# Optimization experiments

Measured on AMD Instinct MI355X. Metric: run time of the kernel, lower is better.

## Reference

```python
import jax, jax.numpy as jnp
import numpy as np

EPS = 1e-06

def quant4(x):
    # per-row (last dim) symmetric 4-bit quant with straight-through estimator
    max_abs = jax.lax.stop_gradient(jnp.max(jnp.abs(x), axis=-1, keepdims=True))
    max_abs = jnp.maximum(max_abs, EPS)
    q = jnp.clip(jnp.round(x / max_abs * 7.0), -8.0, 7.0)
    deq = q * max_abs / 7.0
    # forward value = deq, gradient = identity w.r.t. x
    return x + jax.lax.stop_gradient(deq - x)

def ternary_weight(w):
    thresh = 0.05 * jnp.mean(jnp.abs(w))
    sign = jnp.where(jnp.abs(w) < thresh, 0.0, jnp.sign(w))
    alpha = jnp.mean(jnp.abs(w), axis=1, keepdims=True)  # per output row scale
    tern = sign * alpha
    # forward value = tern, gradient = identity w.r.t. w
    return w + jax.lax.stop_gradient(tern - w)

def setup_inputs() -> dict:
    key = jax.random.key(0)
    kx, kw = jax.random.split(key)
    B, S, IN_F, OUT_F = 8, 4096, 1024, 1024
    x = jax.random.normal(kx, (B, S, IN_F), dtype=jnp.float32)
    weight = jax.random.normal(kw, (OUT_F, IN_F), dtype=jnp.float32) / np.sqrt(IN_F)
    bias = jnp.zeros((OUT_F,), dtype=jnp.float32)
    return {"x": x, "weight": weight, "bias": bias}

def reference(x, weight, bias):
    xq = quant4(x)                       # [B, S, in_f]
    wq = ternary_weight(weight)          # [out_f, in_f]
    out = jnp.einsum('bsi,oi->bso', xq, wq) + bias
    return out
```

## Files before the change

kernel.cpp:

```cpp
#include <hip/hip_runtime.h>
#include <hip/hip_bf16.h>


typedef __attribute__((ext_vector_type(4))) int int32x4;
typedef __attribute__((ext_vector_type(4))) float f32x4;

#define IN_F 1024
#define OUT_F 1024

__device__ inline float waveMax(float v) {
#pragma unroll
    for (int off = 32; off > 0; off >>= 1) v = fmaxf(v, __shfl_xor(v, off, 64));
    return v;
}
__device__ inline float waveSum(float v) {
#pragma unroll
    for (int off = 32; off > 0; off >>= 1) v += __shfl_xor(v, off, 64);
    return v;
}

__device__ inline unsigned int pack4(int a, int b, int c, int d) {
    return (unsigned)(a & 255) | ((unsigned)(b & 255) << 8) |
           ((unsigned)(c & 255) << 16) | ((unsigned)(d & 255) << 24);
}

__global__ __launch_bounds__(256) void wsum_kernel(const float* __restrict__ w,
                                                   float* __restrict__ alpha) {
    __shared__ float red[4];
    const int row = blockIdx.x;
    const int tid = threadIdx.x;
    f32x4 v = reinterpret_cast<const f32x4*>(w + (size_t)row * IN_F)[tid];
    float s = fabsf(v.x) + fabsf(v.y) + fabsf(v.z) + fabsf(v.w);
    s = waveSum(s);
    if ((tid & 63) == 0) red[tid >> 6] = s;
    __syncthreads();
    if (tid == 0)
        alpha[row] = (red[0] + red[1] + red[2] + red[3]) * (1.0f / (float)IN_F);
}

__global__ __launch_bounds__(256) void wquant_kernel(const float* __restrict__ w,
                                                     const float* __restrict__ alpha,
                                                     signed char* __restrict__ wq) {
    __shared__ float red[4];
    const int tid = threadIdx.x;
    f32x4 a = reinterpret_cast<const f32x4*>(alpha)[tid];
    float s = a.x + a.y + a.z + a.w;
    s = waveSum(s);
    if ((tid & 63) == 0) red[tid >> 6] = s;
    __syncthreads();
    const float thresh =
        0.05f * ((red[0] + red[1] + red[2] + red[3]) * (1.0f / (float)OUT_F));

    const int row = blockIdx.x;
    f32x4 v = reinterpret_cast<const f32x4*>(w + (size_t)row * IN_F)[tid];
    int s0 = (fabsf(v.x) < thresh) ? 0 : (v.x > 0.0f ? 1 : -1);
    int s1 = (fabsf(v.y) < thresh) ? 0 : (v.y > 0.0f ? 1 : -1);
    int s2 = (fabsf(v.z) < thresh) ? 0 : (v.z > 0.0f ? 1 : -1);
    int s3 = (fabsf(v.w) < thresh) ? 0 : (v.w > 0.0f ? 1 : -1);
    reinterpret_cast<unsigned int*>(wq)[(size_t)row * (IN_F / 4) + tid] =
        pack4(s0, s1, s2, s3);
}

__global__ __launch_bounds__(256) void quantx_kernel(const float* __restrict__ x,
                                                     signed char* __restrict__ xq,
                                                     float* __restrict__ sx) {
    const int row = blockIdx.x * 4 + (threadIdx.x >> 6);
    const int lane = threadIdx.x & 63;
    const f32x4* xr = reinterpret_cast<const f32x4*>(x + (size_t)row * IN_F);

    f32x4 v[4];
    float m = 0.0f;
#pragma unroll
    for (int j = 0; j < 4; ++j) {
        v[j] = __builtin_nontemporal_load(&xr[lane + 64 * j]);
        m = fmaxf(m, fmaxf(fmaxf(fabsf(v[j].x), fabsf(v[j].y)),
                           fmaxf(fabsf(v[j].z), fabsf(v[j].w))));
    }
    m = waveMax(m);
    m = fmaxf(m, 1e-6f);

    unsigned int* xqr = reinterpret_cast<unsigned int*>(xq + (size_t)row * IN_F);
#pragma unroll
    for (int j = 0; j < 4; ++j) {
        float t0 = fminf(fmaxf(rintf((v[j].x / m) * 7.0f), -8.0f), 7.0f);
        float t1 = fminf(fmaxf(rintf((v[j].y / m) * 7.0f), -8.0f), 7.0f);
        float t2 = fminf(fmaxf(rintf((v[j].z / m) * 7.0f), -8.0f), 7.0f);
        float t3 = fminf(fmaxf(rintf((v[j].w / m) * 7.0f), -8.0f), 7.0f);
        xqr[lane + 64 * j] = pack4((int)t0, (int)t1, (int)t2, (int)t3);
    }
    if (lane == 0) sx[row] = m * (1.0f / 7.0f);
}

__global__ __launch_bounds__(256) void gemm_kernel(
    const signed char* __restrict__ xq, const signed char* __restrict__ wq,
    const float* __restrict__ sx, const float* __restrict__ alpha,
    const float* __restrict__ bias, float* __restrict__ out) {
    const int nwg = gridDim.x;
    int bid = blockIdx.x;
    if ((nwg & 7) == 0) bid = (bid & 7) * (nwg >> 3) + (bid >> 3);
    const int bn = bid & 7;
    const int bm = bid >> 3;

    const int lane = threadIdx.x & 63;
    const int wid = threadIdx.x >> 6;
    const int m_w = bm * 128 + (wid >> 1) * 64;
    const int n_w = bn * 128 + (wid & 1) * 64;
    const int fr = lane & 15;
    const int koff = (lane >> 4) * 16;

    const signed char* ap = xq + (size_t)(m_w + fr) * IN_F + koff;
    const signed char* bp = wq + (size_t)(n_w + fr) * IN_F + koff;

    int32x4 acc[4][4];
#pragma unroll
    for (int i = 0; i < 4; ++i)
#pragma unroll
        for (int j = 0; j < 4; ++j) acc[i][j] = (int32x4){0, 0, 0, 0};

    int32x4 afr[2][4], bfr[2][4];
#pragma unroll
    for (int i = 0; i < 4; ++i)
        afr[0][i] = *reinterpret_cast<const int32x4*>(ap + (size_t)i * 16 * IN_F);
#pragma unroll
    for (int j = 0; j < 4; ++j)
        bfr[0][j] = *reinterpret_cast<const int32x4*>(bp + (size_t)j * 16 * IN_F);

#pragma unroll
    for (int t = 0; t < 16; ++t) {
        const int cur = t & 1, nxt = cur ^ 1;
        if (t < 15) {
            const int k1 = (t + 1) * 64;
#pragma unroll
            for (int i = 0; i < 4; ++i)
                afr[nxt][i] = *reinterpret_cast<const int32x4*>(
                    ap + (size_t)i * 16 * IN_F + k1);
#pragma unroll
            for (int j = 0; j < 4; ++j)
                bfr[nxt][j] = *reinterpret_cast<const int32x4*>(
                    bp + (size_t)j * 16 * IN_F + k1);
        }
#pragma unroll
        for (int i = 0; i < 4; ++i)
#pragma unroll
            for (int j = 0; j < 4; ++j)
                acc[i][j] = __builtin_amdgcn_mfma_i32_16x16x64_i8(
                    afr[cur][i], bfr[cur][j], acc[i][j], 0, 0, 0);
    }

    const int crow = (lane >> 4) * 4;
    const int ccol = lane & 15;
#pragma unroll
    for (int j = 0; j < 4; ++j) {
        const int n = n_w + j * 16 + ccol;
        const float al = alpha[n];
        const float bs = bias[n];
#pragma unroll
        for (int i = 0; i < 4; ++i) {
            const int mbase = m_w + i * 16 + crow;
#pragma unroll
            for (int rr = 0; rr < 4; ++rr) {
                const int m = mbase + rr;
                __builtin_nontemporal_store(
                    (float)acc[i][j][rr] * (sx[m] * al) + bs,
                    &out[(size_t)m * OUT_F + n]);
            }
        }
    }
}

extern "C" void kernel_launch(void* const* d_in, const int* in_sizes, int n_in,
                              void* d_out, int out_size, void* d_ws, size_t ws_size,
                              hipStream_t stream) {
    const float* x = (const float*)d_in[0];
    const float* w = (const float*)d_in[1];
    const float* bias = (const float*)d_in[2];
    float* out = (float*)d_out;
    const int M = in_sizes[0] / IN_F;

    char* ws = (char*)d_ws;
    signed char* xq = (signed char*)ws;
    signed char* wq = xq + (size_t)M * IN_F;
    float* sx = (float*)(wq + (size_t)OUT_F * IN_F);
    float* alpha = sx + M;

    wsum_kernel<<<OUT_F, 256, 0, stream>>>(w, alpha);
    wquant_kernel<<<OUT_F, 256, 0, stream>>>(w, alpha, wq);
    quantx_kernel<<<M / 4, 256, 0, stream>>>(x, xq, sx);
    gemm_kernel<<<(M / 128) * (OUT_F / 128), 256, 0, stream>>>(xq, wq, sx, alpha,
                                                               bias, out);
}
```

Measured before the change: 346.5 us.

## Stage int8 GEMM tiles through LDS with async global_load_lds double buffering

Before, each wave loaded its own A and B MFMA fragments straight from global memory, so every tile row was fetched twice within a workgroup. Now the gemm kernel copies the shared 128x64 A and B tiles into double-buffered LDS with global_load_lds, and all four waves read their fragments from LDS, with one barrier per k-step. This cuts redundant global and L2 traffic, at the cost of a barrier each iteration and reliance on the compiler inserting the right waits for the async LDS copies. The output store also changes from nontemporal to a normal store.

New measurement: 308.3 us. 1.12x faster.

```diff
diff --git a/kernel.cpp b/kernel.cpp
--- a/kernel.cpp
+++ b/kernel.cpp
@@ -22,6 +22,12 @@
 __device__ inline unsigned int pack4(int a, int b, int c, int d) {
     return (unsigned)(a & 255) | ((unsigned)(b & 255) << 8) |
            ((unsigned)(c & 255) << 16) | ((unsigned)(d & 255) << 24);
+}
+
+__device__ inline void gll16(const void* g, void* l) {
+    __builtin_amdgcn_global_load_lds(
+        (const __attribute__((address_space(1))) void*)g,
+        (__attribute__((address_space(3))) void*)l, 16, 0, 0);
 }
 
 __global__ __launch_bounds__(256) void wsum_kernel(const float* __restrict__ w,
@@ -95,21 +101,31 @@
     const signed char* __restrict__ xq, const signed char* __restrict__ wq,
     const float* __restrict__ sx, const float* __restrict__ alpha,
     const float* __restrict__ bias, float* __restrict__ out) {
+    __shared__ signed char lds[2][2][8192];
+
     const int nwg = gridDim.x;
     int bid = blockIdx.x;
     if ((nwg & 7) == 0) bid = (bid & 7) * (nwg >> 3) + (bid >> 3);
     const int bn = bid & 7;
     const int bm = bid >> 3;
+    const int m_b = bm * 128;
+    const int n_b = bn * 128;
 
     const int lane = threadIdx.x & 63;
     const int wid = threadIdx.x >> 6;
-    const int m_w = bm * 128 + (wid >> 1) * 64;
-    const int n_w = bn * 128 + (wid & 1) * 64;
-    const int fr = lane & 15;
-    const int koff = (lane >> 4) * 16;
-
-    const signed char* ap = xq + (size_t)(m_w + fr) * IN_F + koff;
-    const signed char* bp = wq + (size_t)(n_w + fr) * IN_F + koff;
+
+    const int srow = wid * 16 + (lane & 15);
+    const int skb = (lane >> 4) * 16;
+    const signed char* aSrc0 = xq + (size_t)(m_b + srow) * IN_F + skb;
+    const signed char* aSrc1 = xq + (size_t)(m_b + 64 + srow) * IN_F + skb;
+    const signed char* bSrc0 = wq + (size_t)(n_b + srow) * IN_F + skb;
+    const signed char* bSrc1 = wq + (size_t)(n_b + 64 + srow) * IN_F + skb;
+    const int ldsA0 = wid * 1024;
+    const int ldsA1 = 4096 + wid * 1024;
+
+    const int wmh = wid >> 1, wnh = wid & 1;
+    const int aOff = wmh * 4096 + lane * 16;
+    const int bOff = wnh * 4096 + lane * 16;
 
     int32x4 acc[4][4];
 #pragma unroll
@@ -117,36 +133,39 @@
 #pragma unroll
         for (int j = 0; j < 4; ++j) acc[i][j] = (int32x4){0, 0, 0, 0};
 
-    int32x4 afr[2][4], bfr[2][4];
-#pragma unroll
-    for (int i = 0; i < 4; ++i)
-        afr[0][i] = *reinterpret_cast<const int32x4*>(ap + (size_t)i * 16 * IN_F);
-#pragma unroll
-    for (int j = 0; j < 4; ++j)
-        bfr[0][j] = *reinterpret_cast<const int32x4*>(bp + (size_t)j * 16 * IN_F);
+    gll16(aSrc0, &lds[0][0][ldsA0]);
+    gll16(aSrc1, &lds[0][0][ldsA1]);
+    gll16(bSrc0, &lds[0][1][ldsA0]);
+    gll16(bSrc1, &lds[0][1][ldsA1]);
 
 #pragma unroll
     for (int t = 0; t < 16; ++t) {
-        const int cur = t & 1, nxt = cur ^ 1;
+        const int cur = t & 1;
+        __syncthreads();
         if (t < 15) {
             const int k1 = (t + 1) * 64;
-#pragma unroll
-            for (int i = 0; i < 4; ++i)
-                afr[nxt][i] = *reinterpret_cast<const int32x4*>(
-                    ap + (size_t)i * 16 * IN_F + k1);
+            gll16(aSrc0 + k1, &lds[cur ^ 1][0][ldsA0]);
+            gll16(aSrc1 + k1, &lds[cur ^ 1][0][ldsA1]);
+            gll16(bSrc0 + k1, &lds[cur ^ 1][1][ldsA0]);
+            gll16(bSrc1 + k1, &lds[cur ^ 1][1][ldsA1]);
+        }
+        int32x4 afr[4], bfr[4];
+#pragma unroll
+        for (int i = 0; i < 4; ++i)
+            afr[i] = *reinterpret_cast<const int32x4*>(&lds[cur][0][aOff + i * 1024]);
+#pragma unroll
+        for (int j = 0; j < 4; ++j)
+            bfr[j] = *reinterpret_cast<const int32x4*>(&lds[cur][1][bOff + j * 1024]);
+#pragma unroll
+        for (int i = 0; i < 4; ++i)
 #pragma unroll
             for (int j = 0; j < 4; ++j)
-                bfr[nxt][j] = *reinterpret_cast<const int32x4*>(
-                    bp + (size_t)j * 16 * IN_F + k1);
-        }
-#pragma unroll
-        for (int i = 0; i < 4; ++i)
-#pragma unroll
-            for (int j = 0; j < 4; ++j)
-                acc[i][j] = __builtin_amdgcn_mfma_i32_16x16x64_i8(
-                    afr[cur][i], bfr[cur][j], acc[i][j], 0, 0, 0);
-    }
-
+                acc[i][j] = __builtin_amdgcn_mfma_i32_16x16x64_i8(afr[i], bfr[j],
+                                                                  acc[i][j], 0, 0, 0);
+    }
+
+    const int m_w = m_b + wmh * 64;
+    const int n_w = n_b + wnh * 64;
     const int crow = (lane >> 4) * 4;
     const int ccol = lane & 15;
 #pragma unroll
@@ -160,9 +179,7 @@
 #pragma unroll
             for (int rr = 0; rr < 4; ++rr) {
                 const int m = mbase + rr;
-                __builtin_nontemporal_store(
-                    (float)acc[i][j][rr] * (sx[m] * al) + bs,
-                    &out[(size_t)m * OUT_F + n]);
+                out[(size_t)m * OUT_F + n] = (float)acc[i][j][rr] * (sx[m] * al) + bs;
             }
         }
     }
```
